# Performance work log

Hardware: AMD Instinct MI355X
Metric: run time of the kernel (lower is better)

Reference implementation:

```python
import jax, jax.numpy as jnp
import numpy as np
from jax import lax

WINDOW_SIZE = 11
SIGMA = 1.5
C1 = 0.01 ** 2
C2 = 0.03 ** 2


def _gaussian_window(window_size, sigma, channel):
    # 1D gaussian, normalized, then outer product -> 2D window
    x = np.arange(window_size) - window_size // 2
    g = np.exp(-(x.astype(np.float64) ** 2) / (2.0 * sigma ** 2))
    g = (g / g.sum()).astype(np.float32)
    w2d = np.outer(g, g)  # [K, K]
    # depthwise kernel [C, 1, K, K] (OIHW with feature_group_count=C)
    w = np.broadcast_to(w2d, (channel, 1, window_size, window_size))
    return jnp.asarray(np.ascontiguousarray(w))


def _depthwise_conv(x, w, channel):
    pad = WINDOW_SIZE // 2
    return lax.conv_general_dilated(
        x, w,
        window_strides=(1, 1),
        padding=[(pad, pad), (pad, pad)],
        dimension_numbers=("NCHW", "OIHW", "NCHW"),
        feature_group_count=channel,
    )


def setup_inputs() -> dict:
    key = jax.random.key(0)
    k1, k2 = jax.random.split(key)
    B, C, H, W = 32, 3, 512, 512
    img1 = jax.random.uniform(k1, (B, C, H, W), dtype=jnp.float32)
    img2 = jax.random.uniform(k2, (B, C, H, W), dtype=jnp.float32)
    return {"img1": img1, "img2": img2}


def reference(img1, img2):
    channel = img1.shape[1]
    window = _gaussian_window(WINDOW_SIZE, SIGMA, channel)

    mu1 = _depthwise_conv(img1, window, channel)
    mu2 = _depthwise_conv(img2, window, channel)

    mu1_sq = mu1 * mu1
    mu2_sq = mu2 * mu2
    mu1_mu2 = mu1 * mu2

    sigma1_sq = _depthwise_conv(img1 * img1, window, channel) - mu1_sq
    sigma2_sq = _depthwise_conv(img2 * img2, window, channel) - mu2_sq
    sigma12 = _depthwise_conv(img1 * img2, window, channel) - mu1_mu2

    sigma1_sq = jnp.maximum(sigma1_sq, 0.0)
    sigma2_sq = jnp.maximum(sigma2_sq, 0.0)

    numerator = (2.0 * mu1_mu2 + C1) * (2.0 * sigma12 + C2)
    denominator = (mu1_sq + mu2_sq + C1) * (sigma1_sq + sigma2_sq + C2)
    ssim_map = jnp.clip(numerator / denominator, 0.0, 1.0)

    return 1.0 - jnp.mean(ssim_map)
```

## Files before the change

kernel.cpp:

```cpp
#include <hip/hip_runtime.h>


typedef float v2f __attribute__((ext_vector_type(2)));
typedef float v4f __attribute__((ext_vector_type(4)));

constexpr int IMG    = 512;
constexpr int TPB    = 256;
constexpr int SH     = 64;
constexpr int NPAIR  = 37;
constexpr int LW     = 272;
constexpr int PLANES = 32 * 3;
constexpr double N_PIX = 25165824.0;

__global__ __launch_bounds__(TPB) void ssim_map_kernel(
    const float* __restrict__ img1, const float* __restrict__ img2,
    double* __restrict__ partial)
{
    constexpr float GW[11] = {
        0.0010283801f, 0.0075987583f, 0.0360007721f, 0.1093607008f,
        0.2130055439f, 0.2660117257f, 0.2130055439f, 0.1093607008f,
        0.0360007721f, 0.0075987583f, 0.0010283801f };
    constexpr float GWp[13] = {
        0.0f,
        0.0010283801f, 0.0075987583f, 0.0360007721f, 0.1093607008f,
        0.2130055439f, 0.2660117257f, 0.2130055439f, 0.1093607008f,
        0.0360007721f, 0.0075987583f, 0.0010283801f,
        0.0f };

    __shared__ v4f  sbuf[3][LW];
    __shared__ float wsum[TPB / 64];

    const int tid   = threadIdx.x;
    const int x0    = blockIdx.x * TPB;
    const int y0    = blockIdx.y * SH;
    const int plane = blockIdx.z;

    const float* p1 = img1 + (size_t)plane * IMG * IMG;
    const float* p2 = img2 + (size_t)plane * IMG * IMG;

    const int  c   = x0 + tid - 8;
    const bool cok = (unsigned)c < (unsigned)IMG;
    const int  c2  = x0 + 248 + tid;
    const bool c2ok = (unsigned)c2 < (unsigned)IMG;

    v2f rg1[6], rg2[6], rg11[6], rg22[6], rg12[6];

    v2f accv = {0.0f, 0.0f};

    float pa1, pb1, pa2, pb2, qa1, qb1, qa2, qb2;
    auto prefetch = [&](int i) {
        const int  rA  = y0 - 5 + 2 * i;
        const int  rB  = rA + 1;
        const bool aok = (unsigned)rA < (unsigned)IMG;
        const bool bok = (unsigned)rB < (unsigned)IMG;
        const size_t oA = (size_t)rA * IMG;
        const size_t oB = (size_t)rB * IMG;
        pa1 = (aok && cok) ? p1[oA + c] : 0.0f;
        pb1 = (bok && cok) ? p1[oB + c] : 0.0f;
        pa2 = (aok && cok) ? p2[oA + c] : 0.0f;
        pb2 = (bok && cok) ? p2[oB + c] : 0.0f;
        if (tid < 16) {
            qa1 = (aok && c2ok) ? p1[oA + c2] : 0.0f;
            qb1 = (bok && c2ok) ? p1[oB + c2] : 0.0f;
            qa2 = (aok && c2ok) ? p2[oA + c2] : 0.0f;
            qb2 = (bok && c2ok) ? p2[oB + c2] : 0.0f;
        }
    };

    prefetch(0);

    for (int ib = 0; ib < NPAIR; ib += 6) {
#pragma unroll
        for (int j = 0; j < 6; ++j) {
            const int i = ib + j;
            if (i < NPAIR) {
                sbuf[j % 3][tid] = v4f{pa1, pb1, pa2, pb2};
                if (tid < 16) sbuf[j % 3][256 + tid] = v4f{qa1, qb1, qa2, qb2};

                if (i + 1 < NPAIR) prefetch(i + 1);

                __syncthreads();

                v2f a1 = {0,0}, a2 = {0,0}, a11 = {0,0}, a22 = {0,0}, a12 = {0,0};
                const v4f* sp = &sbuf[j % 3][tid + 3];
#pragma unroll
                for (int k = 0; k < 11; ++k) {
                    const v4f s  = sp[k];
                    const v2f x1 = __builtin_shufflevector(s, s, 0, 1);
                    const v2f x2 = __builtin_shufflevector(s, s, 2, 3);
                    const float g = GW[k];
                    const v2f t1 = g * x1;
                    const v2f t2 = g * x2;
                    a1 += t1;
                    a2 += t2;
                    a11 = __builtin_elementwise_fma(t1, x1, a11);
                    a22 = __builtin_elementwise_fma(t2, x2, a22);
                    a12 = __builtin_elementwise_fma(t1, x2, a12);
                }
                rg1[j] = a1;  rg2[j] = a2;
                rg11[j] = a11; rg22[j] = a22; rg12[j] = a12;
            }

            if (i >= 5 && i < NPAIR) {
                v2f sx1={0,0}, sy1={0,0}, sx2={0,0}, sy2={0,0};
                v2f sx11={0,0}, sy11={0,0}, sx22={0,0}, sy22={0,0};
                v2f sx12={0,0}, sy12={0,0};
#pragma unroll
                for (int m = 0; m < 6; ++m) {
                    const int s = (j + 1 + m) % 6;
                    const v2f wx = { GWp[2*m + 1], GWp[2*m + 2] };
                    const v2f wy = { GWp[2*m],     GWp[2*m + 1] };
                    sx1  = __builtin_elementwise_fma(wx, rg1[s],  sx1);
                    sy1  = __builtin_elementwise_fma(wy, rg1[s],  sy1);
                    sx2  = __builtin_elementwise_fma(wx, rg2[s],  sx2);
                    sy2  = __builtin_elementwise_fma(wy, rg2[s],  sy2);
                    sx11 = __builtin_elementwise_fma(wx, rg11[s], sx11);
                    sy11 = __builtin_elementwise_fma(wy, rg11[s], sy11);
                    sx22 = __builtin_elementwise_fma(wx, rg22[s], sx22);
                    sy22 = __builtin_elementwise_fma(wy, rg22[s], sy22);
                    sx12 = __builtin_elementwise_fma(wx, rg12[s], sx12);
                    sy12 = __builtin_elementwise_fma(wy, rg12[s], sy12);
                }
                const v2f m1  = { sx1.x + sx1.y,  sy1.x + sy1.y };
                const v2f m2  = { sx2.x + sx2.y,  sy2.x + sy2.y };
                const v2f e11 = { sx11.x + sx11.y, sy11.x + sy11.y };
                const v2f e22 = { sx22.x + sx22.y, sy22.x + sy22.y };
                const v2f e12 = { sx12.x + sx12.y, sy12.x + sy12.y };

                const v2f mu11 = m1 * m1;
                const v2f mu22 = m2 * m2;
                const v2f mu12 = m1 * m2;
                const v2f zero = {0.0f, 0.0f};
                const v2f one  = {1.0f, 1.0f};
                const v2f sg1  = __builtin_elementwise_max(e11 - mu11, zero);
                const v2f sg2  = __builtin_elementwise_max(e22 - mu22, zero);
                const v2f sg12 = e12 - mu12;
                const v2f num = (2.0f * mu12 + 1e-4f) * (2.0f * sg12 + 9e-4f);
                const v2f den = (mu11 + mu22 + 1e-4f) * (sg1 + sg2 + 9e-4f);
                v2f v = { num.x * __builtin_amdgcn_rcpf(den.x),
                          num.y * __builtin_amdgcn_rcpf(den.y) };
                v = __builtin_elementwise_min(__builtin_elementwise_max(v, zero), one);
                accv += v;
            }
        }
    }

    float acc = accv.x + accv.y;
#pragma unroll
    for (int off = 32; off > 0; off >>= 1)
        acc += __shfl_down(acc, off, 64);
    if ((tid & 63) == 0) wsum[tid >> 6] = acc;
    __syncthreads();
    if (tid == 0) {
        double blocksum = 0.0;
#pragma unroll
        for (int w = 0; w < TPB / 64; ++w) blocksum += (double)wsum[w];
        atomicAdd(partial, blocksum);
    }
}

__global__ void ssim_finalize_kernel(const double* __restrict__ partial,
                                     float* __restrict__ out)
{
    out[0] = 1.0f - (float)(partial[0] / N_PIX);
}

extern "C" void kernel_launch(void* const* d_in, const int* in_sizes, int n_in,
                              void* d_out, int out_size, void* d_ws, size_t ws_size,
                              hipStream_t stream) {
    const float* img1 = (const float*)d_in[0];
    const float* img2 = (const float*)d_in[1];
    float* out = (float*)d_out;
    double* acc = (double*)d_ws;

    hipMemsetAsync(acc, 0, sizeof(double), stream);

    dim3 grid(IMG / TPB, IMG / SH, PLANES);
    ssim_map_kernel<<<grid, TPB, 0, stream>>>(img1, img2, acc);
    ssim_finalize_kernel<<<1, 1, 0, stream>>>(acc, out);
}
```

Before: 256.8 us.

## Give each wavefront its own 64-column strip and drop block barriers

Each 64-lane wavefront now works on an independent 64x64 strip with a private double-buffered LDS row buffer, so the per-row __syncthreads is replaced by a wave-local lgkmcnt wait. The grid is flattened to one dimension and each wave atomically adds its own partial sum. This removes block-wide barrier stalls but raises the halo overhead (10 extra columns per 64 instead of 16 per 256), adds more global loads, and puts four times as many double atomics on the single accumulator. Correctness relies on wave-synchronous LDS visibility plus a two-slot buffer.

```diff
diff --git a/kernel.cpp b/kernel.cpp
--- a/kernel.cpp
+++ b/kernel.cpp
@@ -6,10 +6,15 @@
 
 constexpr int IMG    = 512;
 constexpr int TPB    = 256;
+constexpr int WPB    = 4;
+constexpr int SW     = 64;
 constexpr int SH     = 64;
-constexpr int NPAIR  = 37;
-constexpr int LW     = 272;
+constexpr int NPAIR  = (SH + 10) / 2;
+constexpr int LE     = 80;
+constexpr int NSX    = IMG / SW;
+constexpr int NSY    = IMG / SH;
 constexpr int PLANES = 32 * 3;
+constexpr int NSTRIP = NSX * NSY * PLANES;
 constexpr double N_PIX = 25165824.0;
 
 __global__ __launch_bounds__(TPB) void ssim_map_kernel(
@@ -27,20 +32,26 @@
         0.0360007721f, 0.0075987583f, 0.0010283801f,
         0.0f };
 
-    __shared__ v4f  sbuf[3][LW];
-    __shared__ float wsum[TPB / 64];
+    __shared__ v4f sbuf[WPB][2][LE];
 
-    const int tid   = threadIdx.x;
-    const int x0    = blockIdx.x * TPB;
-    const int y0    = blockIdx.y * SH;
-    const int plane = blockIdx.z;
+    const int tid  = threadIdx.x;
+    const int wid  = tid >> 6;
+    const int lane = tid & 63;
+
+    const int s     = blockIdx.x * WPB + wid;
+    const int xs    = s & (NSX - 1);
+    const int ys    = (s >> 3) & (NSY - 1);
+    const int plane = s >> 6;
+
+    const int x0 = xs * SW;
+    const int y0 = ys * SH;
 
     const float* p1 = img1 + (size_t)plane * IMG * IMG;
     const float* p2 = img2 + (size_t)plane * IMG * IMG;
 
-    const int  c   = x0 + tid - 8;
-    const bool cok = (unsigned)c < (unsigned)IMG;
-    const int  c2  = x0 + 248 + tid;
+    const int  c    = x0 + lane - 5;
+    const bool cok  = (unsigned)c < (unsigned)IMG;
+    const int  c2   = x0 + 59 + lane;
     const bool c2ok = (unsigned)c2 < (unsigned)IMG;
 
     v2f rg1[6], rg2[6], rg11[6], rg22[6], rg12[6];
@@ -59,7 +70,7 @@
         pb1 = (bok && cok) ? p1[oB + c] : 0.0f;
         pa2 = (aok && cok) ? p2[oA + c] : 0.0f;
         pb2 = (bok && cok) ? p2[oB + c] : 0.0f;
-        if (tid < 16) {
+        if (lane < 10) {
             qa1 = (aok && c2ok) ? p1[oA + c2] : 0.0f;
             qb1 = (bok && c2ok) ? p1[oB + c2] : 0.0f;
             qa2 = (aok && c2ok) ? p2[oA + c2] : 0.0f;
@@ -74,20 +85,20 @@
         for (int j = 0; j < 6; ++j) {
             const int i = ib + j;
             if (i < NPAIR) {
-                sbuf[j % 3][tid] = v4f{pa1, pb1, pa2, pb2};
-                if (tid < 16) sbuf[j % 3][256 + tid] = v4f{qa1, qb1, qa2, qb2};
+                const int sl = j & 1;
+                sbuf[wid][sl][lane] = v4f{pa1, pb1, pa2, pb2};
+                if (lane < 10) sbuf[wid][sl][64 + lane] = v4f{qa1, qb1, qa2, qb2};
+                asm volatile("s_waitcnt lgkmcnt(0)" ::: "memory");
 
                 if (i + 1 < NPAIR) prefetch(i + 1);
 
-                __syncthreads();
-
                 v2f a1 = {0,0}, a2 = {0,0}, a11 = {0,0}, a22 = {0,0}, a12 = {0,0};
-                const v4f* sp = &sbuf[j % 3][tid + 3];
+                const v4f* sp = &sbuf[wid][sl][lane];
 #pragma unroll
                 for (int k = 0; k < 11; ++k) {
-                    const v4f s  = sp[k];
-                    const v2f x1 = __builtin_shufflevector(s, s, 0, 1);
-                    const v2f x2 = __builtin_shufflevector(s, s, 2, 3);
+                    const v4f sv = sp[k];
+                    const v2f x1 = __builtin_shufflevector(sv, sv, 0, 1);
+                    const v2f x2 = __builtin_shufflevector(sv, sv, 2, 3);
                     const float g = GW[k];
                     const v2f t1 = g * x1;
                     const v2f t2 = g * x2;
@@ -107,19 +118,19 @@
                 v2f sx12={0,0}, sy12={0,0};
 #pragma unroll
                 for (int m = 0; m < 6; ++m) {
-                    const int s = (j + 1 + m) % 6;
+                    const int sr = (j + 1 + m) % 6;
                     const v2f wx = { GWp[2*m + 1], GWp[2*m + 2] };
                     const v2f wy = { GWp[2*m],     GWp[2*m + 1] };
-                    sx1  = __builtin_elementwise_fma(wx, rg1[s],  sx1);
-                    sy1  = __builtin_elementwise_fma(wy, rg1[s],  sy1);
-                    sx2  = __builtin_elementwise_fma(wx, rg2[s],  sx2);
-                    sy2  = __builtin_elementwise_fma(wy, rg2[s],  sy2);
-                    sx11 = __builtin_elementwise_fma(wx, rg11[s], sx11);
-                    sy11 = __builtin_elementwise_fma(wy, rg11[s], sy11);
-                    sx22 = __builtin_elementwise_fma(wx, rg22[s], sx22);
-                    sy22 = __builtin_elementwise_fma(wy, rg22[s], sy22);
-                    sx12 = __builtin_elementwise_fma(wx, rg12[s], sx12);
-                    sy12 = __builtin_elementwise_fma(wy, rg12[s], sy12);
+                    sx1  = __builtin_elementwise_fma(wx, rg1[sr],  sx1);
+                    sy1  = __builtin_elementwise_fma(wy, rg1[sr],  sy1);
+                    sx2  = __builtin_elementwise_fma(wx, rg2[sr],  sx2);
+                    sy2  = __builtin_elementwise_fma(wy, rg2[sr],  sy2);
+                    sx11 = __builtin_elementwise_fma(wx, rg11[sr], sx11);
+                    sy11 = __builtin_elementwise_fma(wy, rg11[sr], sy11);
+                    sx22 = __builtin_elementwise_fma(wx, rg22[sr], sx22);
+                    sy22 = __builtin_elementwise_fma(wy, rg22[sr], sy22);
+                    sx12 = __builtin_elementwise_fma(wx, rg12[sr], sx12);
+                    sy12 = __builtin_elementwise_fma(wy, rg12[sr], sy12);
                 }
                 const v2f m1  = { sx1.x + sx1.y,  sy1.x + sy1.y };
                 const v2f m2  = { sx2.x + sx2.y,  sy2.x + sy2.y };
@@ -149,14 +160,8 @@
 #pragma unroll
     for (int off = 32; off > 0; off >>= 1)
         acc += __shfl_down(acc, off, 64);
-    if ((tid & 63) == 0) wsum[tid >> 6] = acc;
-    __syncthreads();
-    if (tid == 0) {
-        double blocksum = 0.0;
-#pragma unroll
-        for (int w = 0; w < TPB / 64; ++w) blocksum += (double)wsum[w];
-        atomicAdd(partial, blocksum);
-    }
+    if (lane == 0)
+        atomicAdd(partial, (double)acc);
 }
 
 __global__ void ssim_finalize_kernel(const double* __restrict__ partial,
@@ -175,7 +180,7 @@
 
     hipMemsetAsync(acc, 0, sizeof(double), stream);
 
-    dim3 grid(IMG / TPB, IMG / SH, PLANES);
+    dim3 grid(NSTRIP / WPB);
     ssim_map_kernel<<<grid, TPB, 0, stream>>>(img1, img2, acc);
     ssim_finalize_kernel<<<1, 1, 0, stream>>>(acc, out);
 }
```

New measurement: 273.3 us. 6.4% more time.
